# Kernel optimization log

Hardware: AMD Instinct MI355X
Metric: run time of the kernel (lower is better)

The kernel has to match this reference:

```python
import jax, jax.numpy as jnp
import numpy as np

W_REG = 3.0
N_CAND = 4
IOU_LEN = 15.0
BIG_COST = 1e8


def focal_cost(cls_pred, gt_labels, alpha=0.25, gamma=2.0, eps=1e-12):
    # cls_pred: [B,P,C] logits, gt_labels: [B,T] int -> [B,P,T]
    p = jax.nn.sigmoid(cls_pred)
    neg = -jnp.log(1.0 - p + eps) * (1.0 - alpha) * p ** gamma
    pos = -jnp.log(p + eps) * alpha * (1.0 - p) ** gamma
    B, P, _ = cls_pred.shape
    T = gt_labels.shape[1]
    idx = jnp.broadcast_to(gt_labels[:, None, :], (B, P, T))
    return jnp.take_along_axis(pos, idx, axis=2) - jnp.take_along_axis(neg, idx, axis=2)


def line_iou(pred, target, img_w, length=IOU_LEN):
    # pred: [B,P,O], target: [B,T,O] -> [B,P,T] (unaligned)
    px1, px2 = pred - length, pred + length
    tx1, tx2 = target - length, target + length
    ovr = jnp.minimum(px2[:, :, None, :], tx2[:, None, :, :]) - jnp.maximum(px1[:, :, None, :], tx1[:, None, :, :])
    union = jnp.maximum(px2[:, :, None, :], tx2[:, None, :, :]) - jnp.minimum(px1[:, :, None, :], tx1[:, None, :, :])
    invalid = ((target < 0) | (target >= img_w))[:, None, :, :]
    ovr = jnp.where(invalid, 0.0, ovr)
    union = jnp.where(invalid, 0.0, union)
    return ovr.sum(-1) / (union.sum(-1) + 1e-9)


def clrnet_assign(preds, targets, masks, img_w, img_h):
    B, P, _ = preds.shape
    T = targets.shape[1]
    w = float(img_w - 1)
    h = float(img_h - 1)
    pa = preds.at[..., 3].multiply(w).at[..., 6:].multiply(w)
    ta = targets.at[..., 3].multiply(w).at[..., 6:].multiply(w)
    p_off, t_off = pa[..., 6:], ta[..., 6:]

    # --- distance score (masked mean L1 over valid target x-offsets) ---
    tvalid = (t_off >= 0) & (t_off < img_w)                      # [B,T,O]
    cmask = tvalid[:, None, :, :]                                 # [B,1,T,O]
    clen = jnp.maximum(cmask.sum(-1).astype(pa.dtype), 1.0)      # [B,1,T]
    diff = jnp.abs(p_off[:, :, None, :] - t_off[:, None, :, :]) * cmask  # [B,P,T,O]
    distances = diff.sum(-1) / clen                               # [B,P,T]
    dist_max = jnp.maximum(distances.max(axis=(1, 2), keepdims=True), 1e-8)
    dist_score = 1.0 - distances / dist_max + 0.01

    # --- start-point score (euclidean on (y*(h), x)) ---
    ps = pa[..., 2:4].at[..., 0].multiply(h)
    ts = ta[..., 2:4].at[..., 0].multiply(h)
    start_d = jnp.sqrt(((ps[:, :, None, :] - ts[:, None, :, :]) ** 2).sum(-1))
    start_max = jnp.maximum(start_d.max(axis=(1, 2), keepdims=True), 1e-8)
    start_score = 1.0 - start_d / start_max + 0.01

    # --- theta score ---
    th_d = jnp.abs(pa[..., 4][:, :, None] - ta[..., 4][:, None, :]) * 180.0
    th_max = jnp.maximum(th_d.max(axis=(1, 2), keepdims=True), 1e-8)
    th_score = 1.0 - th_d / th_max + 0.01

    # --- total cost ---
    gt_labels = ta[..., 1].astype(jnp.int32)
    cls_cost = focal_cost(pa[..., :2], gt_labels)
    reg = (jnp.maximum(dist_score, 1e-3) * jnp.maximum(start_score, 1e-3)
           * jnp.maximum(th_score, 1e-3))
    total_cost = -(reg ** 2) * W_REG + cls_cost                   # [B,P,T]
    valid_t = (masks > 0)[:, None, :]                             # [B,1,T]
    total_cost = jnp.where(valid_t, total_cost, BIG_COST)

    # --- dynamic-k from line IoU ---
    liou = jnp.nan_to_num(line_iou(p_off, t_off, img_w), nan=0.0)
    liou = jnp.where(valid_t, liou, 0.0)
    k = min(N_CAND, P)
    topk_ious, _ = jax.lax.top_k(jnp.swapaxes(liou, 1, 2), k)     # [B,T,k]
    dynamic_ks = jnp.maximum(topk_ious.sum(-1).astype(jnp.int32), 1)
    dynamic_ks = jnp.where(masks > 0, dynamic_ks, 0)              # [B,T]

    # --- top-k lowest-cost priors per target, scatter into matching matrix ---
    _, topk_idx = jax.lax.top_k(-jnp.swapaxes(total_cost, 1, 2), k)  # [B,T,k]
    sel = (jnp.arange(k)[None, None, :] < dynamic_ks[:, :, None]).astype(total_cost.dtype)  # [B,T,k]
    one_hot_p = jax.nn.one_hot(topk_idx, P, dtype=total_cost.dtype)  # [B,T,k,P]
    matching = jnp.swapaxes((one_hot_p * sel[..., None]).sum(2), 1, 2)  # [B,P,T]

    # --- conflict resolution: a prior matched to >1 targets keeps argmin-cost one ---
    conflict = matching.sum(-1) > 1                               # [B,P]
    masked_cost = jnp.where(matching == 0, jnp.inf, total_cost)
    best_t = jnp.argmin(masked_cost, axis=2)                      # [B,P]
    new_m = jax.nn.one_hot(best_t, T, dtype=matching.dtype)
    matching = jnp.where(conflict[..., None], new_m, matching)

    has_match = matching.sum(-1) > 0.5
    t_idx = jnp.argmax(matching, axis=2)
    matched = jnp.where(has_match, t_idx, -1).astype(jnp.int32)
    return matched >= 0, matched


def setup_inputs() -> dict:
    key = jax.random.key(0)
    k1, k2, k3 = jax.random.split(key, 3)
    B, P, T, O = 32, 1000, 16, 72
    D = 6 + O
    preds = jax.random.uniform(k1, (B, P, D), dtype=jnp.float32)
    # slightly outside [0,1] so the invalid-offset masking path is exercised
    targets = jax.random.uniform(k2, (B, T, D), dtype=jnp.float32, minval=-0.05, maxval=1.05)
    masks = jax.random.randint(k3, (B, T), 0, 2).astype(jnp.int32)
    return {"preds": preds, "targets": targets, "masks": masks, "img_w": 800, "img_h": 320}


def reference(preds, targets, masks, img_w, img_h):
    return clrnet_assign(preds, targets, masks, img_w, img_h)
```

## Files before the change

kernel.cpp:

```cpp
#include <hip/hip_runtime.h>
#include <math.h>

#define B_ 32
#define P_ 1000
#define T_ 16
#define D_ 78
#define O_ 72
#define NXB 16
#define BIGC 100000000.0f

__global__ __launch_bounds__(1024, 8) void k1(
        const float* __restrict__ preds, const float* __restrict__ targets,
        const int* __restrict__ imgw_p, const int* __restrict__ imgh_p,
        float* __restrict__ dist, float* __restrict__ liou,
        float4* __restrict__ scal4, float* __restrict__ pths,
        float* __restrict__ pmax) {
    __shared__ float pred_s[64 * 81];
    __shared__ float2 tomg[T_ * O_];
    __shared__ float Spart[T_][4][64];
    __shared__ float wmax[16][3];
    __shared__ float cnt_s[T_], clen_s[T_], ts0_s[T_], ts1_s[T_], tth_s[T_];

    const int b = blockIdx.y, bx = blockIdx.x;
    const int p0 = bx * 64;
    const int rows = min(64, P_ - p0);
    const int tid = threadIdx.x;
    const float w = (float)(imgw_p[0] - 1);
    const float h = (float)(imgh_p[0] - 1);
    const float imgwf = (float)imgw_p[0];

    {
        const float4* gbase = (const float4*)(preds + ((size_t)b * P_ + p0) * D_);
        const int n4 = rows * D_ / 4;
        for (int i = tid; i < n4; i += 1024) {
            float4 v = gbase[i];
            int base = i * 4;
            int r = base / D_, c = base - r * D_;
#pragma unroll
            for (int k = 0; k < 4; ++k) {
                int cc = c + k, rr = r;
                if (cc >= D_) { cc -= D_; ++rr; }
                float x = (&v.x)[k];
                if (cc >= 6 || cc == 3) x *= w;
                pred_s[rr * 81 + cc] = x;
            }
        }
    }
    for (int i = tid; i < T_ * O_; i += 1024) {
        int t = i / O_, o = i - t * O_;
        float to = targets[((size_t)b * T_ + t) * D_ + 6 + o] * w;
        float m = (to >= 0.f && to < imgwf) ? 1.f : 0.f;
        tomg[((t >> 2) * O_ + o) * 4 + (t & 3)] = make_float2(to, m);
    }
    __syncthreads();
    if (tid < T_) {
        int t = tid;
        float c = 0.f;
        for (int o = 0; o < O_; ++o) c += tomg[((t >> 2) * O_ + o) * 4 + (t & 3)].y;
        cnt_s[t] = c;
        clen_s[t] = fmaxf(c, 1.f);
        const float* tr = targets + ((size_t)b * T_ + t) * D_;
        ts0_s[t] = tr[2] * h;
        ts1_s[t] = tr[3] * w;
        tth_s[t] = tr[4];
    }
    __syncthreads();

    {
        const int lane = tid & 63;
        const int wv = tid >> 6;
        const int tg = wv & 3;
        const int oq = wv >> 2;
        const float* lrow = pred_s + lane * 81;
        const float4* tg4 = (const float4*)(tomg + (size_t)tg * O_ * 4);
        const int o_lo = oq * 18;
        float S0 = 0.f, S1 = 0.f, S2 = 0.f, S3 = 0.f;
#pragma unroll
        for (int i = 0; i < 18; ++i) {
            int o = o_lo + i;
            float po = lrow[6 + o];
            float4 r0 = tg4[2 * o];
            float4 r1 = tg4[2 * o + 1];
            S0 += r0.y * fabsf(po - r0.x);
            S1 += r0.w * fabsf(po - r0.z);
            S2 += r1.y * fabsf(po - r1.x);
            S3 += r1.w * fabsf(po - r1.z);
        }
        Spart[4 * tg + 0][oq][lane] = S0;
        Spart[4 * tg + 1][oq][lane] = S1;
        Spart[4 * tg + 2][oq][lane] = S2;
        Spart[4 * tg + 3][oq][lane] = S3;
    }
    __syncthreads();

    const int th = tid >> 6, pl = tid & 63;
    const int p = p0 + pl;
    float ldm = 0.f, lsm = 0.f, ltm = 0.f;
    if (pl < rows) {
        float S = ((Spart[th][0][pl] + Spart[th][1][pl]) + Spart[th][2][pl]) + Spart[th][3][pl];
        float dv = S / clen_s[th];
        dist[(size_t)(b * T_ + th) * P_ + p] = dv;
        ldm = dv;
        float c30 = 30.f * cnt_s[th];
        liou[(size_t)(b * T_ + th) * P_ + p] = (c30 - S) / (c30 + S + 1e-9f);
        const float* prow = pred_s + pl * 81;
        float ps0 = prow[2] * h, ps1 = prow[3], pth = prow[4];
        float d0 = ps0 - ts0_s[th], d1 = ps1 - ts1_s[th];
        lsm = sqrtf(d0 * d0 + d1 * d1);
        ltm = fabsf(pth - tth_s[th]) * 180.f;
        if (th == 0) {
            float fc[2];
#pragma unroll
            for (int c = 0; c < 2; ++c) {
                float x = prow[c];
                float pc = 1.f / (1.f + expf(-x));
                float neg = -logf(1.f - pc + 1e-12f) * 0.75f * pc * pc;
                float pos = -logf(pc + 1e-12f) * 0.25f * (1.f - pc) * (1.f - pc);
                fc[c] = pos - neg;
            }
            scal4[(size_t)b * P_ + p] = make_float4(fc[0], fc[1], ps0, ps1);
            pths[(size_t)b * P_ + p] = pth;
        }
    }

    for (int off = 32; off; off >>= 1) {
        ldm = fmaxf(ldm, __shfl_xor(ldm, off, 64));
        lsm = fmaxf(lsm, __shfl_xor(lsm, off, 64));
        ltm = fmaxf(ltm, __shfl_xor(ltm, off, 64));
    }
    if (pl == 0) { wmax[th][0] = ldm; wmax[th][1] = lsm; wmax[th][2] = ltm; }
    __syncthreads();
    if (tid == 0) {
        float m0 = 0.f, m1 = 0.f, m2 = 0.f;
#pragma unroll
        for (int i = 0; i < 16; ++i) {
            m0 = fmaxf(m0, wmax[i][0]);
            m1 = fmaxf(m1, wmax[i][1]);
            m2 = fmaxf(m2, wmax[i][2]);
        }
        float* q = pmax + (size_t)(b * NXB + bx) * 3;
        q[0] = m0; q[1] = m1; q[2] = m2;
    }
}

__global__ __launch_bounds__(1024) void k2(
        const float* __restrict__ targets, const int* __restrict__ masks,
        const int* __restrict__ imgw_p, const int* __restrict__ imgh_p,
        const float* __restrict__ dist, const float* __restrict__ liou,
        const float4* __restrict__ scal4, const float* __restrict__ pths,
        const float* __restrict__ pmax,
        int* __restrict__ out) {
    __shared__ float costL[T_][P_];
    __shared__ int selE[64];

    const int b = blockIdx.x;
    const int tid = threadIdx.x;
    const int t = tid >> 6;
    const int lane = tid & 63;

    float dm = 0.f, sm = 0.f, tm = 0.f;
    for (int i = 0; i < NXB; ++i) {
        const float* q = pmax + (size_t)(b * NXB + i) * 3;
        dm = fmaxf(dm, q[0]); sm = fmaxf(sm, q[1]); tm = fmaxf(tm, q[2]);
    }
    dm = fmaxf(dm, 1e-8f); sm = fmaxf(sm, 1e-8f); tm = fmaxf(tm, 1e-8f);

    const float w = (float)(imgw_p[0] - 1);
    const float h = (float)(imgh_p[0] - 1);
    const float* tr = targets + (size_t)(b * T_ + t) * D_;
    const float ts0 = tr[2] * h, ts1 = tr[3] * w, tth = tr[4];
    int lab = (int)tr[1]; lab = lab < 0 ? 0 : (lab > 1 ? 1 : lab);
    const int mk = masks[b * T_ + t];

    const float* drow = dist + (size_t)(b * T_ + t) * P_;
    const float* lrow = liou + (size_t)(b * T_ + t) * P_;
    const float4* s4b = scal4 + (size_t)b * P_;
    const float* ptb = pths + (size_t)b * P_;

    float lv[16], cv[16];
#pragma unroll
    for (int i = 0; i < 16; ++i) {
        int p = lane + 64 * i;
        if (p < P_) {
            float d = drow[p];
            float4 s4 = s4b[p];
            float pth = ptb[p];
            float dsc = 1.f - d / dm + 0.01f;
            float d0 = s4.z - ts0, d1 = s4.w - ts1;
            float ssc = 1.f - sqrtf(d0 * d0 + d1 * d1) / sm + 0.01f;
            float tsc = 1.f - fabsf(pth - tth) * 180.f / tm + 0.01f;
            float reg = fmaxf(dsc, 1e-3f) * fmaxf(ssc, 1e-3f) * fmaxf(tsc, 1e-3f);
            float c = -(reg * reg) * 3.f + (lab ? s4.y : s4.x);
            if (mk <= 0) c = BIGC;
            costL[t][p] = c;
            cv[i] = c;
            lv[i] = lrow[p];
        } else {
            cv[i] = INFINITY;
            lv[i] = -INFINITY;
        }
    }

    float sum = 0.f;
    for (int r = 0; r < 4; ++r) {
        float bv = -INFINITY; int bi = 0x7fffffff;
#pragma unroll
        for (int i = 0; i < 16; ++i) {
            if (lv[i] > bv) { bv = lv[i]; bi = lane + 64 * i; }
        }
        for (int off = 32; off; off >>= 1) {
            float ov = __shfl_xor(bv, off, 64);
            int oi = __shfl_xor(bi, off, 64);
            if (ov > bv || (ov == bv && oi < bi)) { bv = ov; bi = oi; }
        }
        sum += bv;
#pragma unroll
        for (int i = 0; i < 16; ++i)
            if (bi == lane + 64 * i) lv[i] = -INFINITY;
    }
    int dk = 0;
    if (mk > 0) {
        dk = (int)sum;
        if (dk < 1) dk = 1;
        if (dk > 4) dk = 4;
    }

    int selp[4];
#pragma unroll
    for (int r = 0; r < 4; ++r) {
        float bv = INFINITY; int bi = 0x7fffffff;
#pragma unroll
        for (int i = 0; i < 16; ++i) {
            if (cv[i] < bv) { bv = cv[i]; bi = lane + 64 * i; }
        }
        for (int off = 32; off; off >>= 1) {
            float ov = __shfl_xor(bv, off, 64);
            int oi = __shfl_xor(bi, off, 64);
            if (ov < bv || (ov == bv && oi < bi)) { bv = ov; bi = oi; }
        }
        selp[r] = bi;
#pragma unroll
        for (int i = 0; i < 16; ++i)
            if (bi == lane + 64 * i) cv[i] = INFINITY;
    }

    if (lane == 0) {
#pragma unroll
        for (int j = 0; j < 4; ++j) selE[4 * t + j] = (j < dk) ? selp[j] : -1;
    }
    __syncthreads();

    if (tid < P_) {
        const int p = tid;
        unsigned int m = 0;
#pragma unroll
        for (int t2 = 0; t2 < T_; ++t2) {
            bool hit = (selE[4 * t2] == p) | (selE[4 * t2 + 1] == p) |
                       (selE[4 * t2 + 2] == p) | (selE[4 * t2 + 3] == p);
            if (hit) m |= 1u << t2;
        }
        int matched = -1;
        if (m) {
            if (__popc(m) == 1) {
                matched = __ffs(m) - 1;
            } else {
                float best = INFINITY;
#pragma unroll
                for (int t2 = 0; t2 < T_; ++t2) {
                    if ((m >> t2) & 1u) {
                        float c = costL[t2][p];
                        if (c < best) { best = c; matched = t2; }
                    }
                }
            }
        }
        out[b * P_ + p] = (matched >= 0) ? 1 : 0;
        out[B_ * P_ + b * P_ + p] = matched;
    }
}

extern "C" void kernel_launch(void* const* d_in, const int* in_sizes, int n_in,
                              void* d_out, int out_size, void* d_ws, size_t ws_size,
                              hipStream_t stream) {
    const float* preds   = (const float*)d_in[0];
    const float* targets = (const float*)d_in[1];
    const int*   masks   = (const int*)d_in[2];
    const int*   imgw    = (const int*)d_in[3];
    const int*   imgh    = (const int*)d_in[4];
    int* out = (int*)d_out;

    char* ws = (char*)d_ws;
    const size_t SZ = (size_t)B_ * T_ * P_ * sizeof(float);
    float*  dist  = (float*)ws;
    float*  liou  = (float*)(ws + SZ);
    float4* scal4 = (float4*)(ws + 2 * SZ);
    float*  pths  = (float*)(ws + 2 * SZ + (size_t)B_ * P_ * 16);
    float*  pmax  = (float*)(ws + 2 * SZ + (size_t)B_ * P_ * 20);

    k1<<<dim3(NXB, B_), 1024, 0, stream>>>(preds, targets, imgw, imgh, dist, liou, scal4, pths, pmax);
    k2<<<B_, 1024, 0, stream>>>(targets, masks, imgw, imgh, dist, liou, scal4, pths, pmax, out);
}
```

Before: 36.61 us.

## Restructure k2 cost computation per-prediction and stage liou/cost in shared memory

The cost-matrix stage of k2 is remapped so each thread handles one prediction across all 16 targets. Its scal4 and pths reads now happen once per prediction rather than once per target, and target scalars are staged in shared memory. The liou values are also copied into shared memory. The top-4 selections then read from LDS with a deactivation bitmask instead of keeping 16-element register arrays per lane, which is meant to cut redundant global loads and register pressure. In exchange it adds an extra 64KB shared buffer and a block barrier, and the selection loops now re-read shared memory each round.

```diff
diff --git a/kernel.cpp b/kernel.cpp
--- a/kernel.cpp
+++ b/kernel.cpp
@@ -150,13 +150,14 @@
         const float4* __restrict__ scal4, const float* __restrict__ pths,
         const float* __restrict__ pmax,
         int* __restrict__ out) {
-    __shared__ float costL[T_][P_];
+    __shared__ float costL[T_][1024];
+    __shared__ float liouL[T_][1024];
+    __shared__ float ts0s[T_], ts1s[T_], tths[T_];
+    __shared__ int labs[T_], mks[T_];
     __shared__ int selE[64];
 
     const int b = blockIdx.x;
     const int tid = threadIdx.x;
-    const int t = tid >> 6;
-    const int lane = tid & 63;
 
     float dm = 0.f, sm = 0.f, tm = 0.f;
     for (int i = 0; i < NXB; ++i) {
@@ -167,86 +168,103 @@
 
     const float w = (float)(imgw_p[0] - 1);
     const float h = (float)(imgh_p[0] - 1);
-    const float* tr = targets + (size_t)(b * T_ + t) * D_;
-    const float ts0 = tr[2] * h, ts1 = tr[3] * w, tth = tr[4];
-    int lab = (int)tr[1]; lab = lab < 0 ? 0 : (lab > 1 ? 1 : lab);
-    const int mk = masks[b * T_ + t];
-
-    const float* drow = dist + (size_t)(b * T_ + t) * P_;
-    const float* lrow = liou + (size_t)(b * T_ + t) * P_;
-    const float4* s4b = scal4 + (size_t)b * P_;
-    const float* ptb = pths + (size_t)b * P_;
-
-    float lv[16], cv[16];
-#pragma unroll
-    for (int i = 0; i < 16; ++i) {
-        int p = lane + 64 * i;
-        if (p < P_) {
-            float d = drow[p];
-            float4 s4 = s4b[p];
-            float pth = ptb[p];
+    if (tid < T_) {
+        const float* tr = targets + (size_t)(b * T_ + tid) * D_;
+        ts0s[tid] = tr[2] * h;
+        ts1s[tid] = tr[3] * w;
+        tths[tid] = tr[4];
+        int lab = (int)tr[1];
+        labs[tid] = lab < 0 ? 0 : (lab > 1 ? 1 : lab);
+        mks[tid] = masks[b * T_ + tid];
+    }
+    __syncthreads();
+
+    if (tid < P_) {
+        const int p = tid;
+        float4 s4 = scal4[(size_t)b * P_ + p];
+        float pth = pths[(size_t)b * P_ + p];
+#pragma unroll
+        for (int t = 0; t < T_; ++t) {
+            float d = dist[(size_t)(b * T_ + t) * P_ + p];
+            float li = liou[(size_t)(b * T_ + t) * P_ + p];
             float dsc = 1.f - d / dm + 0.01f;
-            float d0 = s4.z - ts0, d1 = s4.w - ts1;
+            float d0 = s4.z - ts0s[t], d1 = s4.w - ts1s[t];
             float ssc = 1.f - sqrtf(d0 * d0 + d1 * d1) / sm + 0.01f;
-            float tsc = 1.f - fabsf(pth - tth) * 180.f / tm + 0.01f;
+            float tsc = 1.f - fabsf(pth - tths[t]) * 180.f / tm + 0.01f;
             float reg = fmaxf(dsc, 1e-3f) * fmaxf(ssc, 1e-3f) * fmaxf(tsc, 1e-3f);
-            float c = -(reg * reg) * 3.f + (lab ? s4.y : s4.x);
-            if (mk <= 0) c = BIGC;
+            float c = -(reg * reg) * 3.f + (labs[t] ? s4.y : s4.x);
+            if (mks[t] <= 0) c = BIGC;
             costL[t][p] = c;
-            cv[i] = c;
-            lv[i] = lrow[p];
-        } else {
-            cv[i] = INFINITY;
-            lv[i] = -INFINITY;
-        }
-    }
-
-    float sum = 0.f;
-    for (int r = 0; r < 4; ++r) {
-        float bv = -INFINITY; int bi = 0x7fffffff;
-#pragma unroll
-        for (int i = 0; i < 16; ++i) {
-            if (lv[i] > bv) { bv = lv[i]; bi = lane + 64 * i; }
-        }
-        for (int off = 32; off; off >>= 1) {
-            float ov = __shfl_xor(bv, off, 64);
-            int oi = __shfl_xor(bi, off, 64);
-            if (ov > bv || (ov == bv && oi < bi)) { bv = ov; bi = oi; }
-        }
-        sum += bv;
-#pragma unroll
-        for (int i = 0; i < 16; ++i)
-            if (bi == lane + 64 * i) lv[i] = -INFINITY;
-    }
-    int dk = 0;
-    if (mk > 0) {
-        dk = (int)sum;
-        if (dk < 1) dk = 1;
-        if (dk > 4) dk = 4;
-    }
-
-    int selp[4];
-#pragma unroll
-    for (int r = 0; r < 4; ++r) {
-        float bv = INFINITY; int bi = 0x7fffffff;
-#pragma unroll
-        for (int i = 0; i < 16; ++i) {
-            if (cv[i] < bv) { bv = cv[i]; bi = lane + 64 * i; }
-        }
-        for (int off = 32; off; off >>= 1) {
-            float ov = __shfl_xor(bv, off, 64);
-            int oi = __shfl_xor(bi, off, 64);
-            if (ov < bv || (ov == bv && oi < bi)) { bv = ov; bi = oi; }
-        }
-        selp[r] = bi;
-#pragma unroll
-        for (int i = 0; i < 16; ++i)
-            if (bi == lane + 64 * i) cv[i] = INFINITY;
-    }
-
-    if (lane == 0) {
-#pragma unroll
-        for (int j = 0; j < 4; ++j) selE[4 * t + j] = (j < dk) ? selp[j] : -1;
+            liouL[t][p] = li;
+        }
+    } else {
+#pragma unroll
+        for (int t = 0; t < T_; ++t) {
+            costL[t][tid] = INFINITY;
+            liouL[t][tid] = -INFINITY;
+        }
+    }
+    __syncthreads();
+
+    {
+        const int t = tid >> 6;
+        const int lane = tid & 63;
+        const int mk = mks[t];
+
+        unsigned int deact = 0;
+        float sum = 0.f;
+#pragma unroll
+        for (int r = 0; r < 4; ++r) {
+            float bv = -INFINITY; int bi = 0x7fffffff;
+#pragma unroll
+            for (int i = 0; i < 16; ++i) {
+                int idx = lane + 64 * i;
+                float v = liouL[t][idx];
+                if (deact & (1u << i)) v = -INFINITY;
+                if (v > bv || (v == bv && idx < bi)) { bv = v; bi = idx; }
+            }
+            for (int off = 32; off; off >>= 1) {
+                float ov = __shfl_xor(bv, off, 64);
+                int oi = __shfl_xor(bi, off, 64);
+                if (ov > bv || (ov == bv && oi < bi)) { bv = ov; bi = oi; }
+            }
+            sum += bv;
+            if ((bi & 63) == lane) deact |= 1u << (bi >> 6);
+        }
+        int dk = 0;
+        if (mk > 0) {
+            dk = (int)sum;
+            if (dk < 1) dk = 1;
+            if (dk > 4) dk = 4;
+        }
+
+        int sp[4];
+        deact = 0;
+#pragma unroll
+        for (int r = 0; r < 4; ++r) {
+            float bv = INFINITY; int bi = 0x7fffffff;
+#pragma unroll
+            for (int i = 0; i < 16; ++i) {
+                int idx = lane + 64 * i;
+                float v = costL[t][idx];
+                if (deact & (1u << i)) v = INFINITY;
+                if (v < bv || (v == bv && idx < bi)) { bv = v; bi = idx; }
+            }
+            for (int off = 32; off; off >>= 1) {
+                float ov = __shfl_xor(bv, off, 64);
+                int oi = __shfl_xor(bi, off, 64);
+                if (ov < bv || (ov == bv && oi < bi)) { bv = ov; bi = oi; }
+            }
+            sp[r] = bi;
+            if ((bi & 63) == lane) deact |= 1u << (bi >> 6);
+        }
+
+        if (lane == 0) {
+            selE[4 * t + 0] = (dk > 0) ? sp[0] : -1;
+            selE[4 * t + 1] = (dk > 1) ? sp[1] : -1;
+            selE[4 * t + 2] = (dk > 2) ? sp[2] : -1;
+            selE[4 * t + 3] = (dk > 3) ? sp[3] : -1;
+        }
     }
     __syncthreads();
 
```

New measurement: 42.75 us. 16.8% more time.

## Split assignment kernel into per-(batch,target) top-k blocks and a separate resolve kernel

Applied to the files above, without the earlier changes.

Stage two now launches one 256-thread block per (batch, target) pair instead of one 1024-thread block per batch, which gives 512 blocks rather than 32. Cost and IoU rows are staged in shared memory, and a single wavefront runs the top-k selections. The selected indices and their costs go to a small workspace buffer, and a new third kernel resolves conflicts per prior using those stored costs. The aim is to fill more compute units on the device, at the price of an extra launch and a global round-trip for the selections.

```diff
diff --git a/kernel.cpp b/kernel.cpp
--- a/kernel.cpp
+++ b/kernel.cpp
@@ -143,20 +143,19 @@
     }
 }
 
-__global__ __launch_bounds__(1024) void k2(
+__global__ __launch_bounds__(256) void k2(
         const float* __restrict__ targets, const int* __restrict__ masks,
         const int* __restrict__ imgw_p, const int* __restrict__ imgh_p,
         const float* __restrict__ dist, const float* __restrict__ liou,
         const float4* __restrict__ scal4, const float* __restrict__ pths,
         const float* __restrict__ pmax,
-        int* __restrict__ out) {
-    __shared__ float costL[T_][P_];
-    __shared__ int selE[64];
-
-    const int b = blockIdx.x;
+        int4* __restrict__ sel, float4* __restrict__ selc) {
+    __shared__ float costL[1024];
+    __shared__ float liouL[1024];
+
+    const int wid = blockIdx.x;
+    const int b = wid >> 4, t = wid & 15;
     const int tid = threadIdx.x;
-    const int t = tid >> 6;
-    const int lane = tid & 63;
 
     float dm = 0.f, sm = 0.f, tm = 0.f;
     for (int i = 0; i < NXB; ++i) {
@@ -177,10 +176,9 @@
     const float4* s4b = scal4 + (size_t)b * P_;
     const float* ptb = pths + (size_t)b * P_;
 
-    float lv[16], cv[16];
-#pragma unroll
-    for (int i = 0; i < 16; ++i) {
-        int p = lane + 64 * i;
+#pragma unroll
+    for (int i = 0; i < 4; ++i) {
+        int p = tid + 256 * i;
         if (p < P_) {
             float d = drow[p];
             float4 s4 = s4b[p];
@@ -192,21 +190,26 @@
             float reg = fmaxf(dsc, 1e-3f) * fmaxf(ssc, 1e-3f) * fmaxf(tsc, 1e-3f);
             float c = -(reg * reg) * 3.f + (lab ? s4.y : s4.x);
             if (mk <= 0) c = BIGC;
-            costL[t][p] = c;
-            cv[i] = c;
-            lv[i] = lrow[p];
+            costL[p] = c;
+            liouL[p] = lrow[p];
         } else {
-            cv[i] = INFINITY;
-            lv[i] = -INFINITY;
-        }
-    }
+            costL[p] = INFINITY;
+            liouL[p] = -INFINITY;
+        }
+    }
+    __syncthreads();
+    if (tid >= 64) return;
+
+    const int lane = tid;
 
     float sum = 0.f;
     for (int r = 0; r < 4; ++r) {
         float bv = -INFINITY; int bi = 0x7fffffff;
 #pragma unroll
         for (int i = 0; i < 16; ++i) {
-            if (lv[i] > bv) { bv = lv[i]; bi = lane + 64 * i; }
+            int ix = lane + 64 * i;
+            float v = liouL[ix];
+            if (v > bv || (v == bv && ix < bi)) { bv = v; bi = ix; }
         }
         for (int off = 32; off; off >>= 1) {
             float ov = __shfl_xor(bv, off, 64);
@@ -214,9 +217,7 @@
             if (ov > bv || (ov == bv && oi < bi)) { bv = ov; bi = oi; }
         }
         sum += bv;
-#pragma unroll
-        for (int i = 0; i < 16; ++i)
-            if (bi == lane + 64 * i) lv[i] = -INFINITY;
+        if ((bi & 63) == lane) liouL[bi] = -INFINITY;
     }
     int dk = 0;
     if (mk > 0) {
@@ -225,52 +226,56 @@
         if (dk > 4) dk = 4;
     }
 
-    int selp[4];
-#pragma unroll
-    for (int r = 0; r < 4; ++r) {
-        float bv = INFINITY; int bi = 0x7fffffff;
-#pragma unroll
-        for (int i = 0; i < 16; ++i) {
-            if (cv[i] < bv) { bv = cv[i]; bi = lane + 64 * i; }
-        }
-        for (int off = 32; off; off >>= 1) {
-            float ov = __shfl_xor(bv, off, 64);
-            int oi = __shfl_xor(bi, off, 64);
-            if (ov < bv || (ov == bv && oi < bi)) { bv = ov; bi = oi; }
-        }
-        selp[r] = bi;
-#pragma unroll
-        for (int i = 0; i < 16; ++i)
-            if (bi == lane + 64 * i) cv[i] = INFINITY;
-    }
+    int s0, s1, s2, s3;
+    float c0, c1, c2, c3;
+#define ROUNDMIN(sr, cr) {                                                \
+        float bv = INFINITY; int bi = 0x7fffffff;                         \
+        _Pragma("unroll")                                                 \
+        for (int i = 0; i < 16; ++i) {                                    \
+            int ix = lane + 64 * i;                                       \
+            float v = costL[ix];                                          \
+            if (v < bv || (v == bv && ix < bi)) { bv = v; bi = ix; }      \
+        }                                                                 \
+        for (int off = 32; off; off >>= 1) {                              \
+            float ov = __shfl_xor(bv, off, 64);                           \
+            int oi = __shfl_xor(bi, off, 64);                             \
+            if (ov < bv || (ov == bv && oi < bi)) { bv = ov; bi = oi; }   \
+        }                                                                 \
+        sr = bi; cr = bv;                                                 \
+        if ((bi & 63) == lane) costL[bi] = INFINITY; }
+    ROUNDMIN(s0, c0) ROUNDMIN(s1, c1) ROUNDMIN(s2, c2) ROUNDMIN(s3, c3)
+#undef ROUNDMIN
 
     if (lane == 0) {
-#pragma unroll
-        for (int j = 0; j < 4; ++j) selE[4 * t + j] = (j < dk) ? selp[j] : -1;
-    }
-    __syncthreads();
-
-    if (tid < P_) {
-        const int p = tid;
-        unsigned int m = 0;
-#pragma unroll
-        for (int t2 = 0; t2 < T_; ++t2) {
-            bool hit = (selE[4 * t2] == p) | (selE[4 * t2 + 1] == p) |
-                       (selE[4 * t2 + 2] == p) | (selE[4 * t2 + 3] == p);
-            if (hit) m |= 1u << t2;
-        }
+        sel[wid]  = make_int4(dk > 0 ? s0 : -1, dk > 1 ? s1 : -1,
+                              dk > 2 ? s2 : -1, dk > 3 ? s3 : -1);
+        selc[wid] = make_float4(c0, c1, c2, c3);
+    }
+}
+
+__global__ __launch_bounds__(256) void k3(const int* __restrict__ sel,
+                                          const float* __restrict__ selc,
+                                          int* __restrict__ out) {
+    __shared__ int selE[64];
+    __shared__ float selC[64];
+    const int b = blockIdx.y, cx = blockIdx.x;
+    if (threadIdx.x < 64) {
+        selE[threadIdx.x] = sel[b * 64 + threadIdx.x];
+        selC[threadIdx.x] = selc[b * 64 + threadIdx.x];
+    }
+    __syncthreads();
+
+    const int p = cx * 250 + threadIdx.x;
+    if (threadIdx.x < 250) {
         int matched = -1;
-        if (m) {
-            if (__popc(m) == 1) {
-                matched = __ffs(m) - 1;
-            } else {
-                float best = INFINITY;
-#pragma unroll
-                for (int t2 = 0; t2 < T_; ++t2) {
-                    if ((m >> t2) & 1u) {
-                        float c = costL[t2][p];
-                        if (c < best) { best = c; matched = t2; }
-                    }
+        float best = INFINITY;
+#pragma unroll
+        for (int t = 0; t < T_; ++t) {
+#pragma unroll
+            for (int j = 0; j < 4; ++j) {
+                if (selE[4 * t + j] == p) {
+                    float c = selC[4 * t + j];
+                    if (c < best) { best = c; matched = t; }
                 }
             }
         }
@@ -296,7 +301,10 @@
     float4* scal4 = (float4*)(ws + 2 * SZ);
     float*  pths  = (float*)(ws + 2 * SZ + (size_t)B_ * P_ * 16);
     float*  pmax  = (float*)(ws + 2 * SZ + (size_t)B_ * P_ * 20);
+    int4*   sel   = (int4*)(ws + 2 * SZ + (size_t)B_ * P_ * 20 + 8192);
+    float4* selc  = (float4*)(ws + 2 * SZ + (size_t)B_ * P_ * 20 + 16384);
 
     k1<<<dim3(NXB, B_), 1024, 0, stream>>>(preds, targets, imgw, imgh, dist, liou, scal4, pths, pmax);
-    k2<<<B_, 1024, 0, stream>>>(targets, masks, imgw, imgh, dist, liou, scal4, pths, pmax, out);
+    k2<<<B_ * T_, 256, 0, stream>>>(targets, masks, imgw, imgh, dist, liou, scal4, pths, pmax, sel, selc);
+    k3<<<dim3(4, B_), 256, 0, stream>>>((const int*)sel, (const float*)selc, out);
 }
```

New measurement: 34.87 us. 4.7% less time.
